# Performance work log

Measured on AMD Instinct MI355X. Metric: run time of the kernel, lower is better.

## Reference

```python
import jax, jax.numpy as jnp
import numpy as np

N_NODES = 100000
N_EDGES = 1000000
IN_CH = 64
HID = 64
NUM_GRAPHS = 1024


def gcn_conv(x, edge_index, W, b):
    # GCNConv with self-loops and symmetric normalization.
    src, dst = edge_index[0], edge_index[1]
    n = x.shape[0]
    # degree including self-loop
    deg = jax.ops.segment_sum(jnp.ones(src.shape[0], x.dtype), dst, num_segments=n) + 1.0
    dinv = jax.lax.rsqrt(deg)
    xw = x @ W  # [N, out]
    norm = dinv[src] * dinv[dst]  # per-edge 1/sqrt(d_i d_j)
    msg = xw[src] * norm[:, None]  # [E, out] gather + scale
    agg = jax.ops.segment_sum(msg, dst, num_segments=n)
    # self-loop contribution: norm = 1/deg
    return agg + xw / deg[:, None] + b


def setup_inputs() -> dict:
    key = jax.random.key(0)
    k = jax.random.split(key, 8)
    x = jax.random.normal(k[0], (N_NODES, IN_CH), dtype=jnp.float32)
    edge_index = jax.random.randint(k[1], (2, N_EDGES), 0, N_NODES, dtype=jnp.int64)
    batch = jnp.sort(jax.random.randint(k[2], (N_NODES,), 0, NUM_GRAPHS, dtype=jnp.int64))
    s1 = 1.0 / np.sqrt(IN_CH)
    s2 = 1.0 / np.sqrt(HID)
    W1 = jax.random.uniform(k[3], (IN_CH, HID), jnp.float32, -s1, s1)
    b1 = jnp.zeros((HID,), jnp.float32)
    W2 = jax.random.uniform(k[4], (HID, HID), jnp.float32, -s2, s2)
    b2 = jnp.zeros((HID,), jnp.float32)
    Wout = jax.random.uniform(k[5], (HID, 1), jnp.float32, -s2, s2)
    bout = jnp.zeros((1,), jnp.float32)
    return {"x": x, "edge_index": edge_index, "batch": batch,
            "W1": W1, "b1": b1, "W2": W2, "b2": b2, "Wout": Wout, "bout": bout}


def reference(x, edge_index, batch, W1, b1, W2, b2, Wout, bout):
    h = jax.nn.relu(gcn_conv(x, edge_index, W1, b1))
    h = jax.nn.relu(gcn_conv(h, edge_index, W2, b2))
    # global_mean_pool over batch ids
    sums = jax.ops.segment_sum(h, batch, num_segments=NUM_GRAPHS)
    cnt = jax.ops.segment_sum(jnp.ones(h.shape[0], h.dtype), batch, num_segments=NUM_GRAPHS)
    pooled = sums / jnp.maximum(cnt, 1.0)[:, None]  # [G, HID]
    return (pooled @ Wout + bout).reshape(-1)
```

## Files before the change

### kernel.cpp

```cpp
#include <hip/hip_runtime.h>
#include <hip/hip_fp16.h>

#define N_NODES   100000
#define N_EDGES   1000000
#define HID       64
#define NUM_GRAPHS 1024
#define NREP      8
#define CAPA      16
#define CAPB      16
#define NGROUP    (N_NODES / 4)
#define NBINS     196
#define BINCAP    6656
#define EPB       2048

typedef _Float16 h16;

static __device__ __forceinline__ int pack2(float a, float b) {
    union { h16 h[2]; int i; } u;
    u.h[0] = (h16)a; u.h[1] = (h16)b;
    return u.i;
}


__global__ __launch_bounds__(256) void bin_scatter(const int* __restrict__ src,
                                                   const int* __restrict__ dst,
                                                   int* __restrict__ bcnt,
                                                   uint2* __restrict__ ebin) {
    __shared__ int lcnt[NBINS];
    __shared__ int lbase[NBINS];
    int t = threadIdx.x;
    for (int b = t; b < NBINS; b += 256) lcnt[b] = 0;
    __syncthreads();
    int e0 = blockIdx.x * EPB + t;
    int myb[8], myp[8], mys[8], myd[8];
    #pragma unroll
    for (int i = 0; i < 8; i++) {
        int e = e0 + i * 256;
        myb[i] = -1;
        if (e < N_EDGES) {
            int d = dst[e];
            mys[i] = src[e];
            myd[i] = d;
            myb[i] = d >> 9;
            myp[i] = atomicAdd(&lcnt[d >> 9], 1);
        }
    }
    __syncthreads();
    for (int b = t; b < NBINS; b += 256)
        lbase[b] = lcnt[b] ? atomicAdd(&bcnt[b], lcnt[b]) : 0;
    __syncthreads();
    #pragma unroll
    for (int i = 0; i < 8; i++) {
        if (myb[i] >= 0) {
            int pos = lbase[myb[i]] + myp[i];
            if (pos < BINCAP)
                ebin[(size_t)myb[i] * BINCAP + pos] =
                    make_uint2((unsigned)mys[i], (unsigned)myd[i]);
        }
    }
}


__global__ __launch_bounds__(256) void bin_build(const uint2* __restrict__ ebin,
                                                 const int* __restrict__ bcnt,
                                                 int* __restrict__ cnt,
                                                 int* __restrict__ ebufA,
                                                 int* __restrict__ ebufB) {
    __shared__ int cntL[512];
    __shared__ int ldsA[512 * 16];
    int t = threadIdx.x;
    int b = blockIdx.x;
    for (int n = t; n < 512; n += 256) cntL[n] = 0;
    __syncthreads();
    int ne = min(bcnt[b], BINCAP);
    const uint2* ep = ebin + (size_t)b * BINCAP;
    for (int k = t; k < ne; k += 256) {
        uint2 e = ep[k];
        int n = (int)(e.y & 511);
        int p = atomicAdd(&cntL[n], 1);
        if (p < CAPA)             ldsA[n * 16 + p] = (int)e.x;
        else if (p < CAPA + CAPB) ebufB[((size_t)((b << 9) + n)) * 16 + (p - CAPA)] = (int)e.x;
    }
    __syncthreads();
    int4* gA = (int4*)(ebufA + ((size_t)b << 9) * 16);
    const int4* lA = (const int4*)ldsA;
    #pragma unroll
    for (int i = 0; i < 8; i++) {
        int v = t + i * 256;
        if ((b << 9) + (v >> 2) < N_NODES) gA[v] = lA[v];
    }
    for (int n = t; n < 512; n += 256) {
        int node = (b << 9) + n;
        if (node < N_NODES) cnt[node] = cntL[n];
    }
}


__global__ __launch_bounds__(256) void gemm64h(const float* __restrict__ X,
                                               const float* __restrict__ W,
                                               const int* __restrict__ cnt,
                                               h16* __restrict__ Y, int nrows) {
    __shared__ float Wl[4096];
    int t = threadIdx.x;
    #pragma unroll
    for (int i = 0; i < 4; i++) {
        int idx = (t + i * 256) * 4;
        *(float4*)(Wl + idx) = *(const float4*)(W + idx);
    }
    __syncthreads();
    int row  = blockIdx.x * 128 + (t >> 1);
    if (row >= nrows) return;
    int half = t & 1;
    float df = (float)(min(cnt[row], CAPA + CAPB) + 1);
    float sc = rsqrtf(df);
    const float4* xr = (const float4*)(X + (size_t)row * 64);
    float4 acc[8];
    #pragma unroll
    for (int j = 0; j < 8; j++) acc[j] = make_float4(0.f, 0.f, 0.f, 0.f);
    const float* wb = Wl + half * 32;
    #pragma unroll
    for (int k4 = 0; k4 < 16; k4++) {
        float4 xv = xr[k4];
        #pragma unroll
        for (int kk = 0; kk < 4; kk++) {
            float xk = (kk == 0) ? xv.x : (kk == 1) ? xv.y : (kk == 2) ? xv.z : xv.w;
            const float4* wr = (const float4*)(wb + (k4 * 4 + kk) * 64);
            #pragma unroll
            for (int j = 0; j < 8; j++) {
                float4 wv = wr[j];
                acc[j].x += xk * wv.x;
                acc[j].y += xk * wv.y;
                acc[j].z += xk * wv.z;
                acc[j].w += xk * wv.w;
            }
        }
    }
    int4* yr = (int4*)(Y + (size_t)row * 64 + half * 32);
    #pragma unroll
    for (int j = 0; j < 4; j++) {
        float4 a = acc[2 * j], b = acc[2 * j + 1];
        int4 o;
        o.x = pack2(a.x * sc, a.y * sc); o.y = pack2(a.z * sc, a.w * sc);
        o.z = pack2(b.x * sc, b.y * sc); o.w = pack2(b.z * sc, b.w * sc);
        yr[j] = o;
    }
}


template <int U>
static __device__ __forceinline__ float agg_chunk(const h16* __restrict__ XW,
                                                  int es, int j, int lane) {
    int ss[U]; float vv[U];
    #pragma unroll
    for (int u = 0; u < U; u++) ss[u] = __builtin_amdgcn_readlane(es, j + u);
    #pragma unroll
    for (int u = 0; u < U; u++)
        vv[u] = (float)XW[(((unsigned)ss[u]) << 6) | (unsigned)lane];
    float a = 0.f;
    #pragma unroll
    for (int u = 0; u < U; u++) a += vv[u];
    return a;
}

static __device__ __forceinline__ float half_agg(const h16* __restrict__ XW,
                                                 int es, int d, int base, int lane) {
    if (d == 16) return agg_chunk<16>(XW, es, base, lane);
    float acc = 0.f;
    int j = 0;
    if (d & 8) { acc += agg_chunk<8>(XW, es, base + j, lane); j += 8; }
    if (d & 4) { acc += agg_chunk<4>(XW, es, base + j, lane); j += 4; }
    if (d & 2) { acc += agg_chunk<2>(XW, es, base + j, lane); j += 2; }
    if (d & 1) { acc += agg_chunk<1>(XW, es, base + j, lane); }
    return acc;
}

static __device__ __forceinline__ float agg_node(const h16* __restrict__ XW,
                                                 int esA, int esB, int deg,
                                                 int base, int lane) {
    float acc = half_agg(XW, esA, min(deg, 16), base, lane);
    if (deg > 16) acc += half_agg(XW, esB, deg - 16, base, lane);
    return acc;
}

__global__ __launch_bounds__(256) void agg_gemm_relu(const h16* __restrict__ XW,
                                                     const int* __restrict__ cnt,
                                                     const int* __restrict__ ebufA,
                                                     const int* __restrict__ ebufB,
                                                     const float* __restrict__ bias,
                                                     const float* __restrict__ W2,
                                                     h16* __restrict__ Y2) {
    __shared__ float W2q[4096];
    __shared__ float hbuf[1024];
    int t = threadIdx.x;
    #pragma unroll
    for (int i = 0; i < 4; i++) {
        int L0 = (t + i * 256) * 4;
        float4 wv = *(const float4*)(W2 + L0);
        int k = L0 >> 6, c = L0 & 63;
        float* dp = &W2q[(k >> 2) * 256 + (k & 3)];
        dp[(c + 0) * 4] = wv.x;
        dp[(c + 1) * 4] = wv.y;
        dp[(c + 2) * 4] = wv.z;
        dp[(c + 3) * 4] = wv.w;
    }
    __syncthreads();
    int lane = t & 63;
    int w = t >> 6;
    float* hb = hbuf + w * 256;
    float bl = bias[lane];
    int gw = blockIdx.x * 4 + w;
    int   esA = ebufA[gw * 64 + lane];
    int   esB = ebufB[gw * 64 + lane];
    float s0 = (float)XW[gw * 256 + lane];
    float s1 = (float)XW[gw * 256 + 64 + lane];
    float s2 = (float)XW[gw * 256 + 128 + lane];
    float s3 = (float)XW[gw * 256 + 192 + lane];
    int4  c4  = *(const int4*)(cnt + 4 * gw);
    int d0 = min(__builtin_amdgcn_readfirstlane(c4.x), CAPA + CAPB);
    int d1 = min(__builtin_amdgcn_readfirstlane(c4.y), CAPA + CAPB);
    int d2 = min(__builtin_amdgcn_readfirstlane(c4.z), CAPA + CAPB);
    int d3 = min(__builtin_amdgcn_readfirstlane(c4.w), CAPA + CAPB);
    float v0 = rsqrtf((float)(d0 + 1));
    float v1 = rsqrtf((float)(d1 + 1));
    float v2 = rsqrtf((float)(d2 + 1));
    float v3 = rsqrtf((float)(d3 + 1));
    float a0 = s0 + agg_node(XW, esA, esB, d0, 0,  lane);
    float a1 = s1 + agg_node(XW, esA, esB, d1, 16, lane);
    float a2 = s2 + agg_node(XW, esA, esB, d2, 32, lane);
    float a3 = s3 + agg_node(XW, esA, esB, d3, 48, lane);
    hb[lane]       = fmaxf(fmaf(v0, a0, bl), 0.f);
    hb[64 + lane]  = fmaxf(fmaf(v1, a1, bl), 0.f);
    hb[128 + lane] = fmaxf(fmaf(v2, a2, bl), 0.f);
    hb[192 + lane] = fmaxf(fmaf(v3, a3, bl), 0.f);
    float y0 = 0.f, y1 = 0.f, y2 = 0.f, y3 = 0.f;
    #pragma unroll
    for (int k4 = 0; k4 < 16; k4++) {
        float4 wq = *(const float4*)(W2q + k4 * 256 + lane * 4);
        float4 h0 = *(const float4*)(hb + k4 * 4);
        float4 h1 = *(const float4*)(hb + 64 + k4 * 4);
        float4 h2 = *(const float4*)(hb + 128 + k4 * 4);
        float4 h3 = *(const float4*)(hb + 192 + k4 * 4);
        y0 = fmaf(h0.x, wq.x, y0); y1 = fmaf(h1.x, wq.x, y1);
        y2 = fmaf(h2.x, wq.x, y2); y3 = fmaf(h3.x, wq.x, y3);
        y0 = fmaf(h0.y, wq.y, y0); y1 = fmaf(h1.y, wq.y, y1);
        y2 = fmaf(h2.y, wq.y, y2); y3 = fmaf(h3.y, wq.y, y3);
        y0 = fmaf(h0.z, wq.z, y0); y1 = fmaf(h1.z, wq.z, y1);
        y2 = fmaf(h2.z, wq.z, y2); y3 = fmaf(h3.z, wq.z, y3);
        y0 = fmaf(h0.w, wq.w, y0); y1 = fmaf(h1.w, wq.w, y1);
        y2 = fmaf(h2.w, wq.w, y2); y3 = fmaf(h3.w, wq.w, y3);
    }
    Y2[gw * 256 + lane]       = (h16)(y0 * v0);
    Y2[gw * 256 + 64 + lane]  = (h16)(y1 * v1);
    Y2[gw * 256 + 128 + lane] = (h16)(y2 * v2);
    Y2[gw * 256 + 192 + lane] = (h16)(y3 * v3);
}

__global__ __launch_bounds__(256) void agg_pool(const h16* __restrict__ XW,
                                                const int* __restrict__ cnt,
                                                const int* __restrict__ ebufA,
                                                const int* __restrict__ ebufB,
                                                const float* __restrict__ bias,
                                                const float* __restrict__ Wout,
                                                const int* __restrict__ batch,
                                                float* __restrict__ outsum) {
    int t = threadIdx.x;
    int lane = t & 63;
    int w = t >> 6;
    float bl = bias[lane];
    float wl = Wout[lane];
    int gw = blockIdx.x * 4 + w;
    int   esA = ebufA[gw * 64 + lane];
    int   esB = ebufB[gw * 64 + lane];
    float s0 = (float)XW[gw * 256 + lane];
    float s1 = (float)XW[gw * 256 + 64 + lane];
    float s2 = (float)XW[gw * 256 + 128 + lane];
    float s3 = (float)XW[gw * 256 + 192 + lane];
    int4  c4  = *(const int4*)(cnt + 4 * gw);
    int4  b4  = *(const int4*)(batch + 4 * gw);
    int d0 = min(__builtin_amdgcn_readfirstlane(c4.x), CAPA + CAPB);
    int d1 = min(__builtin_amdgcn_readfirstlane(c4.y), CAPA + CAPB);
    int d2 = min(__builtin_amdgcn_readfirstlane(c4.z), CAPA + CAPB);
    int d3 = min(__builtin_amdgcn_readfirstlane(c4.w), CAPA + CAPB);
    float vs0 = rsqrtf((float)(d0 + 1));
    float vs1 = rsqrtf((float)(d1 + 1));
    float vs2 = rsqrtf((float)(d2 + 1));
    float vs3 = rsqrtf((float)(d3 + 1));
    float a0 = s0 + agg_node(XW, esA, esB, d0, 0,  lane);
    float a1 = s1 + agg_node(XW, esA, esB, d1, 16, lane);
    float a2 = s2 + agg_node(XW, esA, esB, d2, 32, lane);
    float a3 = s3 + agg_node(XW, esA, esB, d3, 48, lane);
    float v0 = fmaxf(fmaf(vs0, a0, bl), 0.f) * wl;
    float v1 = fmaxf(fmaf(vs1, a1, bl), 0.f) * wl;
    float v2 = fmaxf(fmaf(vs2, a2, bl), 0.f) * wl;
    float v3 = fmaxf(fmaf(vs3, a3, bl), 0.f) * wl;
    #pragma unroll
    for (int off = 32; off > 0; off >>= 1) {
        v0 += __shfl_down(v0, off, 64);
        v1 += __shfl_down(v1, off, 64);
        v2 += __shfl_down(v2, off, 64);
        v3 += __shfl_down(v3, off, 64);
    }
    if (lane == 0) {
        int n0 = 4 * gw;
        atomicAdd(&outsum[((n0 + 0) & (NREP - 1)) * NUM_GRAPHS + b4.x], v0);
        atomicAdd(&outsum[((n0 + 1) & (NREP - 1)) * NUM_GRAPHS + b4.y], v1);
        atomicAdd(&outsum[((n0 + 2) & (NREP - 1)) * NUM_GRAPHS + b4.z], v2);
        atomicAdd(&outsum[((n0 + 3) & (NREP - 1)) * NUM_GRAPHS + b4.w], v3);
    }
}

__global__ __launch_bounds__(256) void finalize(const float* __restrict__ outsum,
                                                const int* __restrict__ batch,
                                                const float* __restrict__ bout,
                                                float* __restrict__ out) {
    int g = blockIdx.x * 256 + threadIdx.x;
    if (g >= NUM_GRAPHS) return;
    float s = 0.f;
    #pragma unroll
    for (int r = 0; r < NREP; r++) s += outsum[r * NUM_GRAPHS + g];
    int lo = 0, hi = N_NODES;
    while (lo < hi) { int mid = (lo + hi) >> 1; if (batch[mid] <  g) lo = mid + 1; else hi = mid; }
    int lo2 = lo, hi2 = N_NODES;
    while (lo2 < hi2) { int mid = (lo2 + hi2) >> 1; if (batch[mid] <= g) lo2 = mid + 1; else hi2 = mid; }
    float c = (float)max(lo2 - lo, 1);
    out[g] = s / c + bout[0];
}


extern "C" void kernel_launch(void* const* d_in, const int* in_sizes, int n_in,
                              void* d_out, int out_size, void* d_ws, size_t ws_size,
                              hipStream_t stream) {
    const float* x     = (const float*)d_in[0];
    const int*   eidx  = (const int*)d_in[1];
    const int*   batch = (const int*)d_in[2];
    const float* W1    = (const float*)d_in[3];
    const float* b1    = (const float*)d_in[4];
    const float* W2    = (const float*)d_in[5];
    const float* b2    = (const float*)d_in[6];
    const float* Wout  = (const float*)d_in[7];
    const float* bout  = (const float*)d_in[8];
    float* out = (float*)d_out;

    const int* src = eidx;
    const int* dst = eidx + N_EDGES;

    h16*   xw     = (h16*)d_ws;
    h16*   y2     = xw + (size_t)N_NODES * 64;
    int*   ebufA  = (int*)(y2 + (size_t)N_NODES * 64);
    int*   ebufB  = ebufA + (size_t)N_NODES * CAPA;
    int*   cnt    = ebufB + (size_t)N_NODES * CAPB;
    float* outsum = (float*)(cnt + N_NODES);
    int*   bcnt   = (int*)(outsum + NREP * NUM_GRAPHS);
    uint2* ebin   = (uint2*)(bcnt + NBINS);

    hipMemsetAsync(outsum, 0, (size_t)(NREP * NUM_GRAPHS + NBINS) * sizeof(int), stream);

    const int SB  = (N_EDGES + EPB - 1) / EPB;
    const int GB  = (N_NODES + 127) / 128;
    const int AGB = NGROUP / 4;

    bin_scatter<<<SB, 256, 0, stream>>>(src, dst, bcnt, ebin);
    bin_build<<<NBINS, 256, 0, stream>>>(ebin, bcnt, cnt, ebufA, ebufB);
    gemm64h<<<GB, 256, 0, stream>>>(x, W1, cnt, xw, N_NODES);
    agg_gemm_relu<<<AGB, 256, 0, stream>>>(xw, cnt, ebufA, ebufB, b1, W2, y2);
    agg_pool<<<AGB, 256, 0, stream>>>(y2, cnt, ebufA, ebufB, b2, Wout, batch, outsum);
    finalize<<<(NUM_GRAPHS + 255) / 256, 256, 0, stream>>>(outsum, batch, bout, out);
}
```

Before: 216.3 us.

## Gather neighbor rows as packed half2 words with two edges per wavefront

The aggregation in both GCN kernels now reads each neighbor row as 32 packed 32-bit half2 words instead of 64 separate halves. The two wave halves process alternating edges of each pair, and their partial sums are combined with a cross-half shuffle. This halves the number of gather instructions per edge and makes each load wider. In exchange it adds shuffle and unpack work, wastes half the wave on the odd tail edge, and changes the pooling reduction to a 32-lane shuffle.

Result: slower. 221.9 us (+2.6%).

```diff
diff --git a/kernel.cpp b/kernel.cpp
--- a/kernel.cpp
+++ b/kernel.cpp
@@ -19,6 +19,14 @@
     union { h16 h[2]; int i; } u;
     u.h[0] = (h16)a; u.h[1] = (h16)b;
     return u.i;
+}
+static __device__ __forceinline__ float lo_h(int v) {
+    union { unsigned short u; h16 h; } c; c.u = (unsigned short)(v & 0xffff);
+    return (float)c.h;
+}
+static __device__ __forceinline__ float hi_h(int v) {
+    union { unsigned short u; h16 h; } c; c.u = (unsigned short)(((unsigned)v) >> 16);
+    return (float)c.h;
 }
 
 
@@ -148,38 +156,56 @@
 
 
 template <int U>
-static __device__ __forceinline__ float agg_chunk(const h16* __restrict__ XW,
-                                                  int es, int j, int lane) {
-    int ss[U]; float vv[U];
-    #pragma unroll
-    for (int u = 0; u < U; u++) ss[u] = __builtin_amdgcn_readlane(es, j + u);
+static __device__ __forceinline__ void pair_chunk_pk(const int* __restrict__ XW32,
+                                                     int es, int jb, int laneq,
+                                                     bool up, float& s0, float& s1) {
+    int sel[U]; int vv[U];
+    #pragma unroll
+    for (int u = 0; u < U; u++) {
+        int sa = __builtin_amdgcn_readlane(es, jb + 2 * u);
+        int sb = __builtin_amdgcn_readlane(es, jb + 2 * u + 1);
+        sel[u] = up ? sb : sa;
+    }
     #pragma unroll
     for (int u = 0; u < U; u++)
-        vv[u] = (float)XW[(((unsigned)ss[u]) << 6) | (unsigned)lane];
-    float a = 0.f;
-    #pragma unroll
-    for (int u = 0; u < U; u++) a += vv[u];
-    return a;
-}
-
-static __device__ __forceinline__ float half_agg(const h16* __restrict__ XW,
-                                                 int es, int d, int base, int lane) {
-    if (d == 16) return agg_chunk<16>(XW, es, base, lane);
-    float acc = 0.f;
-    int j = 0;
-    if (d & 8) { acc += agg_chunk<8>(XW, es, base + j, lane); j += 8; }
-    if (d & 4) { acc += agg_chunk<4>(XW, es, base + j, lane); j += 4; }
-    if (d & 2) { acc += agg_chunk<2>(XW, es, base + j, lane); j += 2; }
-    if (d & 1) { acc += agg_chunk<1>(XW, es, base + j, lane); }
-    return acc;
-}
-
-static __device__ __forceinline__ float agg_node(const h16* __restrict__ XW,
-                                                 int esA, int esB, int deg,
-                                                 int base, int lane) {
-    float acc = half_agg(XW, esA, min(deg, 16), base, lane);
-    if (deg > 16) acc += half_agg(XW, esB, deg - 16, base, lane);
-    return acc;
+        vv[u] = XW32[(((unsigned)sel[u]) << 5) | (unsigned)laneq];
+    #pragma unroll
+    for (int u = 0; u < U; u++) { s0 += lo_h(vv[u]); s1 += hi_h(vv[u]); }
+}
+
+static __device__ __forceinline__ void pair_tail_pk(const int* __restrict__ XW32,
+                                                    int es, int j, int laneq,
+                                                    bool up, float& s0, float& s1) {
+    int s = __builtin_amdgcn_readlane(es, j);
+    int v = XW32[(((unsigned)s) << 5) | (unsigned)laneq];
+    if (!up) { s0 += lo_h(v); s1 += hi_h(v); }
+}
+
+static __device__ __forceinline__ void half_pk(const int* __restrict__ XW32,
+                                               int es, int d, int base, int laneq,
+                                               bool up, float& s0, float& s1) {
+    int P = d >> 1;
+    int j = base;
+    if (P & 8) { pair_chunk_pk<8>(XW32, es, j, laneq, up, s0, s1); j += 16; }
+    if (P & 4) { pair_chunk_pk<4>(XW32, es, j, laneq, up, s0, s1); j += 8; }
+    if (P & 2) { pair_chunk_pk<2>(XW32, es, j, laneq, up, s0, s1); j += 4; }
+    if (P & 1) { pair_chunk_pk<1>(XW32, es, j, laneq, up, s0, s1); j += 2; }
+    if (d & 1) pair_tail_pk(XW32, es, j, laneq, up, s0, s1);
+}
+
+static __device__ __forceinline__ float2 agg_node_pk(const int* __restrict__ XW32,
+                                                     int esA, int esB, int deg,
+                                                     int base, int laneq, bool up) {
+    float s0 = 0.f, s1 = 0.f;
+    half_pk(XW32, esA, min(deg, 16), base, laneq, up, s0, s1);
+    if (deg > 16) half_pk(XW32, esB, deg - 16, base, laneq, up, s0, s1);
+    return make_float2(s0, s1);
+}
+
+static __device__ __forceinline__ float2 finish_pk(float2 e, int selfdw) {
+    float a0 = e.x + __shfl_xor(e.x, 32, 64) + lo_h(selfdw);
+    float a1 = e.y + __shfl_xor(e.y, 32, 64) + hi_h(selfdw);
+    return make_float2(a0, a1);
 }
 
 __global__ __launch_bounds__(256) void agg_gemm_relu(const h16* __restrict__ XW,
@@ -205,17 +231,20 @@
     }
     __syncthreads();
     int lane = t & 63;
+    int laneq = lane & 31;
+    bool up = lane >= 32;
     int w = t >> 6;
     float* hb = hbuf + w * 256;
-    float bl = bias[lane];
+    float2 bl2 = *(const float2*)(bias + 2 * laneq);
     int gw = blockIdx.x * 4 + w;
-    int   esA = ebufA[gw * 64 + lane];
-    int   esB = ebufB[gw * 64 + lane];
-    float s0 = (float)XW[gw * 256 + lane];
-    float s1 = (float)XW[gw * 256 + 64 + lane];
-    float s2 = (float)XW[gw * 256 + 128 + lane];
-    float s3 = (float)XW[gw * 256 + 192 + lane];
-    int4  c4  = *(const int4*)(cnt + 4 * gw);
+    const int* XW32 = (const int*)XW;
+    int esA = ebufA[gw * 64 + lane];
+    int esB = ebufB[gw * 64 + lane];
+    int sd0 = XW32[gw * 128 + laneq];
+    int sd1 = XW32[gw * 128 + 32 + laneq];
+    int sd2 = XW32[gw * 128 + 64 + laneq];
+    int sd3 = XW32[gw * 128 + 96 + laneq];
+    int4 c4 = *(const int4*)(cnt + 4 * gw);
     int d0 = min(__builtin_amdgcn_readfirstlane(c4.x), CAPA + CAPB);
     int d1 = min(__builtin_amdgcn_readfirstlane(c4.y), CAPA + CAPB);
     int d2 = min(__builtin_amdgcn_readfirstlane(c4.z), CAPA + CAPB);
@@ -224,14 +253,22 @@
     float v1 = rsqrtf((float)(d1 + 1));
     float v2 = rsqrtf((float)(d2 + 1));
     float v3 = rsqrtf((float)(d3 + 1));
-    float a0 = s0 + agg_node(XW, esA, esB, d0, 0,  lane);
-    float a1 = s1 + agg_node(XW, esA, esB, d1, 16, lane);
-    float a2 = s2 + agg_node(XW, esA, esB, d2, 32, lane);
-    float a3 = s3 + agg_node(XW, esA, esB, d3, 48, lane);
-    hb[lane]       = fmaxf(fmaf(v0, a0, bl), 0.f);
-    hb[64 + lane]  = fmaxf(fmaf(v1, a1, bl), 0.f);
-    hb[128 + lane] = fmaxf(fmaf(v2, a2, bl), 0.f);
-    hb[192 + lane] = fmaxf(fmaf(v3, a3, bl), 0.f);
+    float2 e0 = agg_node_pk(XW32, esA, esB, d0, 0,  laneq, up);
+    float2 e1 = agg_node_pk(XW32, esA, esB, d1, 16, laneq, up);
+    float2 e2 = agg_node_pk(XW32, esA, esB, d2, 32, laneq, up);
+    float2 e3 = agg_node_pk(XW32, esA, esB, d3, 48, laneq, up);
+    float2 a0 = finish_pk(e0, sd0);
+    float2 a1 = finish_pk(e1, sd1);
+    float2 a2 = finish_pk(e2, sd2);
+    float2 a3 = finish_pk(e3, sd3);
+    *(float2*)(hb +       2 * laneq) = make_float2(fmaxf(fmaf(v0, a0.x, bl2.x), 0.f),
+                                                   fmaxf(fmaf(v0, a0.y, bl2.y), 0.f));
+    *(float2*)(hb +  64 + 2 * laneq) = make_float2(fmaxf(fmaf(v1, a1.x, bl2.x), 0.f),
+                                                   fmaxf(fmaf(v1, a1.y, bl2.y), 0.f));
+    *(float2*)(hb + 128 + 2 * laneq) = make_float2(fmaxf(fmaf(v2, a2.x, bl2.x), 0.f),
+                                                   fmaxf(fmaf(v2, a2.y, bl2.y), 0.f));
+    *(float2*)(hb + 192 + 2 * laneq) = make_float2(fmaxf(fmaf(v3, a3.x, bl2.x), 0.f),
+                                                   fmaxf(fmaf(v3, a3.y, bl2.y), 0.f));
     float y0 = 0.f, y1 = 0.f, y2 = 0.f, y3 = 0.f;
     #pragma unroll
     for (int k4 = 0; k4 < 16; k4++) {
@@ -265,18 +302,21 @@
                                                 float* __restrict__ outsum) {
     int t = threadIdx.x;
     int lane = t & 63;
+    int laneq = lane & 31;
+    bool up = lane >= 32;
     int w = t >> 6;
-    float bl = bias[lane];
-    float wl = Wout[lane];
+    float2 bl2 = *(const float2*)(bias + 2 * laneq);
+    float2 wl2 = *(const float2*)(Wout + 2 * laneq);
     int gw = blockIdx.x * 4 + w;
-    int   esA = ebufA[gw * 64 + lane];
-    int   esB = ebufB[gw * 64 + lane];
-    float s0 = (float)XW[gw * 256 + lane];
-    float s1 = (float)XW[gw * 256 + 64 + lane];
-    float s2 = (float)XW[gw * 256 + 128 + lane];
-    float s3 = (float)XW[gw * 256 + 192 + lane];
-    int4  c4  = *(const int4*)(cnt + 4 * gw);
-    int4  b4  = *(const int4*)(batch + 4 * gw);
+    const int* XW32 = (const int*)XW;
+    int esA = ebufA[gw * 64 + lane];
+    int esB = ebufB[gw * 64 + lane];
+    int sd0 = XW32[gw * 128 + laneq];
+    int sd1 = XW32[gw * 128 + 32 + laneq];
+    int sd2 = XW32[gw * 128 + 64 + laneq];
+    int sd3 = XW32[gw * 128 + 96 + laneq];
+    int4 c4 = *(const int4*)(cnt + 4 * gw);
+    int4 b4 = *(const int4*)(batch + 4 * gw);
     int d0 = min(__builtin_amdgcn_readfirstlane(c4.x), CAPA + CAPB);
     int d1 = min(__builtin_amdgcn_readfirstlane(c4.y), CAPA + CAPB);
     int d2 = min(__builtin_amdgcn_readfirstlane(c4.z), CAPA + CAPB);
@@ -285,20 +325,28 @@
     float vs1 = rsqrtf((float)(d1 + 1));
     float vs2 = rsqrtf((float)(d2 + 1));
     float vs3 = rsqrtf((float)(d3 + 1));
-    float a0 = s0 + agg_node(XW, esA, esB, d0, 0,  lane);
-    float a1 = s1 + agg_node(XW, esA, esB, d1, 16, lane);
-    float a2 = s2 + agg_node(XW, esA, esB, d2, 32, lane);
-    float a3 = s3 + agg_node(XW, esA, esB, d3, 48, lane);
-    float v0 = fmaxf(fmaf(vs0, a0, bl), 0.f) * wl;
-    float v1 = fmaxf(fmaf(vs1, a1, bl), 0.f) * wl;
-    float v2 = fmaxf(fmaf(vs2, a2, bl), 0.f) * wl;
-    float v3 = fmaxf(fmaf(vs3, a3, bl), 0.f) * wl;
-    #pragma unroll
-    for (int off = 32; off > 0; off >>= 1) {
-        v0 += __shfl_down(v0, off, 64);
-        v1 += __shfl_down(v1, off, 64);
-        v2 += __shfl_down(v2, off, 64);
-        v3 += __shfl_down(v3, off, 64);
+    float2 e0 = agg_node_pk(XW32, esA, esB, d0, 0,  laneq, up);
+    float2 e1 = agg_node_pk(XW32, esA, esB, d1, 16, laneq, up);
+    float2 e2 = agg_node_pk(XW32, esA, esB, d2, 32, laneq, up);
+    float2 e3 = agg_node_pk(XW32, esA, esB, d3, 48, laneq, up);
+    float2 a0 = finish_pk(e0, sd0);
+    float2 a1 = finish_pk(e1, sd1);
+    float2 a2 = finish_pk(e2, sd2);
+    float2 a3 = finish_pk(e3, sd3);
+    float v0 = fmaxf(fmaf(vs0, a0.x, bl2.x), 0.f) * wl2.x
+             + fmaxf(fmaf(vs0, a0.y, bl2.y), 0.f) * wl2.y;
+    float v1 = fmaxf(fmaf(vs1, a1.x, bl2.x), 0.f) * wl2.x
+             + fmaxf(fmaf(vs1, a1.y, bl2.y), 0.f) * wl2.y;
+    float v2 = fmaxf(fmaf(vs2, a2.x, bl2.x), 0.f) * wl2.x
+             + fmaxf(fmaf(vs2, a2.y, bl2.y), 0.f) * wl2.y;
+    float v3 = fmaxf(fmaf(vs3, a3.x, bl2.x), 0.f) * wl2.x
+             + fmaxf(fmaf(vs3, a3.y, bl2.y), 0.f) * wl2.y;
+    #pragma unroll
+    for (int off = 16; off > 0; off >>= 1) {
+        v0 += __shfl_down(v0, off, 32);
+        v1 += __shfl_down(v1, off, 32);
+        v2 += __shfl_down(v2, off, 32);
+        v3 += __shfl_down(v3, off, 32);
     }
     if (lane == 0) {
         int n0 = 4 * gw;
```
